# Optimization experiments

Measured on AMD Instinct MI355X. Metric: run time of the kernel, lower is better.

The kernel has to match this reference:

```python
import jax, jax.numpy as jnp
import numpy as np

B, N_FIELDS, D_IN, HID, HEADS = 1024, 32, 64, 128, 4
E_PER_G = 256
N_TOTAL = B * N_FIELDS


def setup_inputs() -> dict:
    key = jax.random.key(0)
    ks = jax.random.split(key, 12)
    # per-graph template edges, replicated with per-graph node offsets
    src_t = jax.random.randint(ks[0], (E_PER_G,), 0, N_FIELDS)
    dst_t = jax.random.randint(ks[1], (E_PER_G,), 0, N_FIELDS)
    offs = (jnp.arange(B) * N_FIELDS)[:, None]
    src = (src_t[None, :] + offs).reshape(-1)
    dst = (dst_t[None, :] + offs).reshape(-1)
    loops = jnp.arange(N_TOTAL)  # PyG GATConv add_self_loops=True
    edge_index = jnp.stack([jnp.concatenate([src, loops]),
                            jnp.concatenate([dst, loops])]).astype(jnp.int32)
    batch_idx = jnp.repeat(jnp.arange(B), N_FIELDS).astype(jnp.int32)

    def glorot(k, shape):
        fan = shape[0]
        return jax.random.normal(k, shape, jnp.float32) / np.float32(np.sqrt(fan))

    return {
        "x_fields": jax.random.normal(ks[2], (B, N_FIELDS, D_IN), jnp.float32),
        "aligner_w": glorot(ks[3], (D_IN, HID)),
        "aligner_b": jnp.zeros((HID,), jnp.float32),
        "ln_gamma": jnp.ones((HID,), jnp.float32),
        "ln_beta": jnp.zeros((HID,), jnp.float32),
        "gate_logits": jnp.full((N_FIELDS,), 2.2, jnp.float32),
        "w1": glorot(ks[4], (HID, HEADS * HID)),
        "att_src1": jax.random.normal(ks[5], (HEADS, HID), jnp.float32) * 0.1,
        "att_dst1": jax.random.normal(ks[6], (HEADS, HID), jnp.float32) * 0.1,
        "bias1": jnp.zeros((HEADS * HID,), jnp.float32),
        "w2": glorot(ks[7], (HEADS * HID, HID)),
        "att_src2": jax.random.normal(ks[8], (1, HID), jnp.float32) * 0.1,
        "att_dst2": jax.random.normal(ks[9], (1, HID), jnp.float32) * 0.1,
        "bias2": jnp.zeros((HID,), jnp.float32),
        "edge_index": edge_index,
        "batch_idx": batch_idx,
    }


def _gat(x, W, a_src, a_dst, bias, src, dst, heads, out_dim, concat):
    n = x.shape[0]
    h = (x @ W).reshape(n, heads, out_dim)          # [N,H,F]
    e_s = jnp.einsum('nhf,hf->nh', h, a_src)         # per-node src logits
    e_d = jnp.einsum('nhf,hf->nh', h, a_dst)
    logits = jax.nn.leaky_relu(e_s[src] + e_d[dst], 0.2)   # [E,H]
    # segment softmax over destination nodes (self-loops -> no empty segs)
    m = jax.ops.segment_max(logits, dst, num_segments=n)
    ex = jnp.exp(logits - m[dst])
    denom = jax.ops.segment_sum(ex, dst, num_segments=n)
    alpha = ex / denom[dst]
    out = jax.ops.segment_sum(h[src] * alpha[..., None], dst, num_segments=n)
    out = out.reshape(n, heads * out_dim) if concat else out.mean(axis=1)
    return out + bias


def reference(x_fields, aligner_w, aligner_b, ln_gamma, ln_beta, gate_logits,
              w1, att_src1, att_dst1, bias1, w2, att_src2, att_dst2, bias2,
              edge_index, batch_idx):
    # fused alignment: one Linear over all fields
    aligned = x_fields @ aligner_w + aligner_b       # [B,N,HID]
    mu = aligned.mean(-1, keepdims=True)
    var = ((aligned - mu) ** 2).mean(-1, keepdims=True)
    normed = (aligned - mu) / jnp.sqrt(var + 1e-5) * ln_gamma + ln_beta
    gate = jax.nn.sigmoid(gate_logits)               # [N]
    x = (normed * gate[None, :, None]).reshape(-1, HID)  # [B*N, HID]
    src, dst = edge_index[0], edge_index[1]
    x = _gat(x, w1, att_src1, att_dst1, bias1, src, dst, HEADS, HID, True)
    x = jax.nn.elu(x)
    x = _gat(x, w2, att_src2, att_dst2, bias2, src, dst, 1, HID, False)
    counts = jax.ops.segment_sum(jnp.ones((x.shape[0],), x.dtype), batch_idx,
                                 num_segments=B)
    graph_embedding = jax.ops.segment_sum(x, batch_idx, num_segments=B) / counts[:, None]
    return graph_embedding, gate
```

## Files before the change

kernel.cpp:

```cpp
#include <hip/hip_runtime.h>
#include <hip/hip_bf16.h>
#include <cstdint>
#include <cstddef>

#define NB    1024
#define NF    32
#define DIN   64
#define HID   128
#define HEADS 4
#define NTOT  (NB*NF)
#define H1DIM (HEADS*HID)

typedef __attribute__((ext_vector_type(8))) short          bf16x8;
typedef __attribute__((ext_vector_type(8))) unsigned short u16x8;
typedef __attribute__((ext_vector_type(4))) float          f32x4;

__device__ __forceinline__ float bf2f(unsigned short u) {
    return __uint_as_float(((unsigned)u) << 16);
}
__device__ __forceinline__ unsigned short f2bf(float f) {
    unsigned u = __float_as_uint(f);
    return (unsigned short)((u + 0x7FFF + ((u >> 16) & 1)) >> 16);
}

__global__ __launch_bounds__(256) void k_prep(
    const float* __restrict__ w1, const float* __restrict__ w2,
    const float* __restrict__ Wa,
    unsigned short* __restrict__ w1T, unsigned short* __restrict__ w2T,
    unsigned short* __restrict__ WaT)
{
    int i = blockIdx.x * 256 + threadIdx.x;
    if (i < HID * H1DIM) {
        int n = i >> 7, k = i & 127;
        w1T[i] = f2bf(w1[k * H1DIM + n]);
    } else if (i < 2 * HID * H1DIM) {
        int j = i - HID * H1DIM;
        int n = j >> 9, k = j & 511;
        w2T[j] = f2bf(w2[k * HID + n]);
    } else {
        int j = i - 2 * HID * H1DIM;
        int c = j >> 6, k = j & 63;
        WaT[j] = f2bf(Wa[k * HID + c]);
    }
}

__global__ __launch_bounds__(256, 2) void k_mega(
    const float* __restrict__ xf, const unsigned short* __restrict__ WaT,
    const float* __restrict__ ba, const float* __restrict__ gamma,
    const float* __restrict__ beta, const float* __restrict__ gl,
    const unsigned short* __restrict__ w1T, const float* __restrict__ as1,
    const float* __restrict__ ad1, const float* __restrict__ b1,
    const unsigned short* __restrict__ w2T, const float* __restrict__ as2,
    const float* __restrict__ ad2, const float* __restrict__ b2,
    const int* __restrict__ src, const int* __restrict__ dst, int epg,
    float* __restrict__ dout)
{
    __shared__ char S[72192];
    unsigned short* h1T    = (unsigned short*)S;
    unsigned short* x1L    = (unsigned short*)S;
    unsigned short* alphaL = (unsigned short*)(S + 40960);
    unsigned short* x0L    = (unsigned short*)(S + 51200);
    int*   cntL  = (int*)  (S + 59904);
    float* lnS   = (float*)(S + 64000);
    float* lnS2  = (float*)(S + 64512);
    float* esL   = (float*)(S + 65024);
    float* edL   = (float*)(S + 65536);
    float* rsumL = (float*)(S + 66048);
    float* es2p  = (float*)(S + 66560);
    float* ed2p  = (float*)(S + 67072);
    float* aL2   = (float*)(S + 67584);
    float* sc2   = (float*)(S + 71808);

    const int b = blockIdx.x, t = threadIdx.x;
    const int l = t & 63, w = t >> 6;
    const int g = l >> 4, i16 = l & 15;
    const int nb = b * NF;
    const f32x4 zf4 = {0.f, 0.f, 0.f, 0.f};

    for (int i = t; i < NF * NF; i += 256) cntL[i] = 0;
    __syncthreads();
    for (int i = t; i < epg; i += 256) {
        int sv = src[b * epg + i] - nb;
        int dv = dst[b * epg + i] - nb;
        atomicAdd(&cntL[dv * NF + sv], 1);
    }
    if (t < NF) atomicAdd(&cntL[t * NF + t], 1);

    f32x4 accA[2][2];
    #pragma unroll
    for (int m = 0; m < 2; ++m)
        #pragma unroll
        for (int n = 0; n < 2; ++n) accA[m][n] = zf4;

    #pragma unroll
    for (int k = 0; k < 2; ++k) {
        bf16x8 aF[2];
        #pragma unroll
        for (int m = 0; m < 2; ++m) {
            const float* p = &xf[(size_t)(nb + m * 16 + i16) * DIN + k * 32 + g * 8];
            float4 f0 = *(const float4*)p;
            float4 f1 = *(const float4*)(p + 4);
            u16x8 v;
            v[0] = f2bf(f0.x); v[1] = f2bf(f0.y); v[2] = f2bf(f0.z); v[3] = f2bf(f0.w);
            v[4] = f2bf(f1.x); v[5] = f2bf(f1.y); v[6] = f2bf(f1.z); v[7] = f2bf(f1.w);
            aF[m] = (bf16x8)v;
        }
        #pragma unroll
        for (int n = 0; n < 2; ++n) {
            bf16x8 bF = *(const bf16x8*)&WaT[(size_t)(w * 32 + n * 16 + i16) * DIN + k * 32 + g * 8];
            #pragma unroll
            for (int m = 0; m < 2; ++m)
                accA[m][n] = __builtin_amdgcn_mfma_f32_16x16x32_bf16(aF[m], bF, accA[m][n], 0, 0, 0);
        }
    }
    float val[2][2][4];
    float bav[2];
    #pragma unroll
    for (int n = 0; n < 2; ++n) bav[n] = ba[w * 32 + n * 16 + i16];
    float ps[2][4], ps2[2][4];
    #pragma unroll
    for (int m = 0; m < 2; ++m)
        #pragma unroll
        for (int v = 0; v < 4; ++v) {
            float a0 = accA[m][0][v] + bav[0];
            float a1 = accA[m][1][v] + bav[1];
            val[m][0][v] = a0; val[m][1][v] = a1;
            ps[m][v] = a0 + a1;
            ps2[m][v] = a0 * a0 + a1 * a1;
        }
    #pragma unroll
    for (int o = 1; o < 16; o <<= 1) {
        #pragma unroll
        for (int m = 0; m < 2; ++m)
            #pragma unroll
            for (int v = 0; v < 4; ++v) {
                ps[m][v]  += __shfl_xor(ps[m][v], o);
                ps2[m][v] += __shfl_xor(ps2[m][v], o);
            }
    }
    if (i16 == 0) {
        #pragma unroll
        for (int m = 0; m < 2; ++m)
            #pragma unroll
            for (int v = 0; v < 4; ++v) {
                int r = m * 16 + g * 4 + v;
                lnS[w * 32 + r]  = ps[m][v];
                lnS2[w * 32 + r] = ps2[m][v];
            }
    }
    __syncthreads();
    #pragma unroll
    for (int m = 0; m < 2; ++m)
        #pragma unroll
        for (int v = 0; v < 4; ++v) {
            int r = m * 16 + g * 4 + v;
            float S1 = lnS[r] + lnS[32 + r] + lnS[64 + r] + lnS[96 + r];
            float S2 = lnS2[r] + lnS2[32 + r] + lnS2[64 + r] + lnS2[96 + r];
            float mu = S1 * (1.0f / HID);
            float var = S2 * (1.0f / HID) - mu * mu;
            float rs = rsqrtf(var + 1e-5f);
            float gt = 1.0f / (1.0f + __expf(-gl[r]));
            #pragma unroll
            for (int n = 0; n < 2; ++n) {
                int c = w * 32 + n * 16 + i16;
                float xv = ((val[m][n][v] - mu) * rs * gamma[c] + beta[c]) * gt;
                x0L[r * 136 + c] = f2bf(xv);
            }
        }
    __syncthreads();

    f32x4 acc1[2][8];
    #pragma unroll
    for (int m = 0; m < 2; ++m)
        #pragma unroll
        for (int n = 0; n < 8; ++n) acc1[m][n] = zf4;

    #pragma unroll 1
    for (int k = 0; k < 4; ++k) {
        bf16x8 aF[2];
        #pragma unroll
        for (int m = 0; m < 2; ++m)
            aF[m] = *(const bf16x8*)&x0L[(m * 16 + i16) * 136 + k * 32 + g * 8];
        #pragma unroll
        for (int n = 0; n < 8; ++n) {
            bf16x8 bF = *(const bf16x8*)&w1T[(size_t)(w * 128 + n * 16 + i16) * 128 + k * 32 + g * 8];
            #pragma unroll
            for (int m = 0; m < 2; ++m)
                acc1[m][n] = __builtin_amdgcn_mfma_f32_16x16x32_bf16(aF[m], bF, acc1[m][n], 0, 0, 0);
        }
    }
    {
        float asv[8], adv[8];
        #pragma unroll
        for (int n = 0; n < 8; ++n) {
            int f = n * 16 + i16;
            asv[n] = as1[w * 128 + f];
            adv[n] = ad1[w * 128 + f];
        }
        float pe[2][4], pd[2][4];
        #pragma unroll
        for (int m = 0; m < 2; ++m)
            #pragma unroll
            for (int v = 0; v < 4; ++v) {
                float e = 0.f, d = 0.f;
                #pragma unroll
                for (int n = 0; n < 8; ++n) {
                    e = fmaf(acc1[m][n][v], asv[n], e);
                    d = fmaf(acc1[m][n][v], adv[n], d);
                }
                pe[m][v] = e; pd[m][v] = d;
            }
        #pragma unroll
        for (int o = 1; o < 16; o <<= 1) {
            #pragma unroll
            for (int m = 0; m < 2; ++m)
                #pragma unroll
                for (int v = 0; v < 4; ++v) {
                    pe[m][v] += __shfl_xor(pe[m][v], o);
                    pd[m][v] += __shfl_xor(pd[m][v], o);
                }
        }
        if (i16 == 0) {
            #pragma unroll
            for (int m = 0; m < 2; ++m)
                #pragma unroll
                for (int v = 0; v < 4; ++v) {
                    int r = m * 16 + g * 4 + v;
                    esL[w * 32 + r] = pe[m][v];
                    edL[w * 32 + r] = pd[m][v];
                }
        }
        #pragma unroll
        for (int m = 0; m < 2; ++m)
            #pragma unroll
            for (int n = 0; n < 8; ++n) {
                int c = w * 128 + n * 16 + i16;
                unsigned d0 = (unsigned)f2bf(acc1[m][n][0]) | ((unsigned)f2bf(acc1[m][n][1]) << 16);
                unsigned d1 = (unsigned)f2bf(acc1[m][n][2]) | ((unsigned)f2bf(acc1[m][n][3]) << 16);
                uint2 pk = {d0, d1};
                *(uint2*)&h1T[c * 40 + m * 16 + g * 4] = pk;
            }
    }
    __syncthreads();

    if (t < 128) {
        int d = t >> 2, h = t & 3;
        float edv = edL[h * 32 + d];
        float mx = -INFINITY;
        #pragma unroll
        for (int s = 0; s < NF; ++s) {
            if (cntL[d * NF + s]) {
                float lg = esL[h * 32 + s] + edv;
                lg = fmaxf(lg, 0.2f * lg);
                mx = fmaxf(mx, lg);
            }
        }
        float sum = 0.f;
        #pragma unroll
        for (int s = 0; s < NF; ++s) {
            int c = cntL[d * NF + s];
            float a = 0.f;
            if (c) {
                float lg = esL[h * 32 + s] + edv;
                lg = fmaxf(lg, 0.2f * lg);
                a = (float)c * __expf(lg - mx);
                sum += a;
            }
            alphaL[(h * 32 + d) * 40 + s] = f2bf(a);
        }
        rsumL[h * 32 + d] = 1.0f / sum;
    }
    __syncthreads();

    f32x4 po[2][8];
    {
        bf16x8 aF2[2];
        #pragma unroll
        for (int m = 0; m < 2; ++m)
            aF2[m] = *(const bf16x8*)&alphaL[(w * 32 + m * 16 + i16) * 40 + g * 8];
        #pragma unroll
        for (int n = 0; n < 8; ++n) {
            bf16x8 bF = *(const bf16x8*)&h1T[(w * 128 + n * 16 + i16) * 40 + g * 8];
            #pragma unroll
            for (int m = 0; m < 2; ++m)
                po[m][n] = __builtin_amdgcn_mfma_f32_16x16x32_bf16(aF2[m], bF, zf4, 0, 0, 0);
        }
    }
    __syncthreads();
    #pragma unroll
    for (int m = 0; m < 2; ++m)
        #pragma unroll
        for (int n = 0; n < 8; ++n) {
            int c = w * 128 + n * 16 + i16;
            float bias = b1[c];
            #pragma unroll
            for (int v = 0; v < 4; ++v) {
                int r = m * 16 + g * 4 + v;
                float x = po[m][n][v] * rsumL[w * 32 + r] + bias;
                x = (x > 0.f) ? x : expm1f(x);
                x1L[r * 520 + c] = f2bf(x);
            }
        }
    __syncthreads();

    f32x4 acc2[2][2];
    #pragma unroll
    for (int m = 0; m < 2; ++m)
        #pragma unroll
        for (int n = 0; n < 2; ++n) acc2[m][n] = zf4;

    #pragma unroll 1
    for (int k = 0; k < 16; ++k) {
        bf16x8 aF[2];
        #pragma unroll
        for (int m = 0; m < 2; ++m)
            aF[m] = *(const bf16x8*)&x1L[(m * 16 + i16) * 520 + k * 32 + g * 8];
        #pragma unroll
        for (int n = 0; n < 2; ++n) {
            bf16x8 bF = *(const bf16x8*)&w2T[(size_t)(w * 32 + n * 16 + i16) * 512 + k * 32 + g * 8];
            #pragma unroll
            for (int m = 0; m < 2; ++m)
                acc2[m][n] = __builtin_amdgcn_mfma_f32_16x16x32_bf16(aF[m], bF, acc2[m][n], 0, 0, 0);
        }
    }
    {
        float a2v[2], d2v[2];
        #pragma unroll
        for (int n = 0; n < 2; ++n) {
            int c = w * 32 + n * 16 + i16;
            a2v[n] = as2[c]; d2v[n] = ad2[c];
        }
        float pe[2][4], pd[2][4];
        #pragma unroll
        for (int m = 0; m < 2; ++m)
            #pragma unroll
            for (int v = 0; v < 4; ++v) {
                float e = 0.f, d = 0.f;
                #pragma unroll
                for (int n = 0; n < 2; ++n) {
                    e = fmaf(acc2[m][n][v], a2v[n], e);
                    d = fmaf(acc2[m][n][v], d2v[n], d);
                }
                pe[m][v] = e; pd[m][v] = d;
            }
        #pragma unroll
        for (int o = 1; o < 16; o <<= 1) {
            #pragma unroll
            for (int m = 0; m < 2; ++m)
                #pragma unroll
                for (int v = 0; v < 4; ++v) {
                    pe[m][v] += __shfl_xor(pe[m][v], o);
                    pd[m][v] += __shfl_xor(pd[m][v], o);
                }
        }
        if (i16 == 0) {
            #pragma unroll
            for (int m = 0; m < 2; ++m)
                #pragma unroll
                for (int v = 0; v < 4; ++v) {
                    int r = m * 16 + g * 4 + v;
                    es2p[w * 32 + r] = pe[m][v];
                    ed2p[w * 32 + r] = pd[m][v];
                }
        }
    }
    __syncthreads();

    float* es2L = sc2;
    float* ed2L = sc2 + 32;
    float* wn2  = sc2 + 64;
    if (t < NF) {
        es2L[t] = es2p[t] + es2p[32 + t] + es2p[64 + t] + es2p[96 + t];
        ed2L[t] = ed2p[t] + ed2p[32 + t] + ed2p[64 + t] + ed2p[96 + t];
    }
    __syncthreads();
    if (t < NF) {
        int d = t;
        float edv = ed2L[d];
        float mx = -INFINITY;
        #pragma unroll
        for (int s = 0; s < NF; ++s) {
            if (cntL[d * NF + s]) {
                float lg = es2L[s] + edv;
                lg = fmaxf(lg, 0.2f * lg);
                mx = fmaxf(mx, lg);
            }
        }
        float sum = 0.f;
        #pragma unroll
        for (int s = 0; s < NF; ++s) {
            int c = cntL[d * NF + s];
            float a = 0.f;
            if (c) {
                float lg = es2L[s] + edv;
                lg = fmaxf(lg, 0.2f * lg);
                a = (float)c * __expf(lg - mx);
                sum += a;
            }
            aL2[d * 33 + s] = a;
        }
        float rs = 1.0f / sum;
        #pragma unroll
        for (int s = 0; s < NF; ++s) aL2[d * 33 + s] *= rs;
    }
    __syncthreads();
    if (t < NF) {
        float a = 0.f;
        #pragma unroll
        for (int d = 0; d < NF; ++d) a += aL2[d * 33 + t];
        wn2[t] = a;
    }
    __syncthreads();

    {
        float wr_[2][4];
        #pragma unroll
        for (int m = 0; m < 2; ++m)
            #pragma unroll
            for (int v = 0; v < 4; ++v) wr_[m][v] = wn2[m * 16 + g * 4 + v];
        float pl[2];
        #pragma unroll
        for (int n = 0; n < 2; ++n) {
            float a = 0.f;
            #pragma unroll
            for (int m = 0; m < 2; ++m)
                #pragma unroll
                for (int v = 0; v < 4; ++v)
                    a = fmaf(wr_[m][v], acc2[m][n][v], a);
            pl[n] = a;
        }
        #pragma unroll
        for (int n = 0; n < 2; ++n) {
            pl[n] += __shfl_xor(pl[n], 16);
            pl[n] += __shfl_xor(pl[n], 32);
        }
        if (l < 16) {
            #pragma unroll
            for (int n = 0; n < 2; ++n) {
                int c = w * 32 + n * 16 + l;
                dout[(size_t)b * HID + c] = pl[n] * (1.0f / NF) + b2[c];
            }
        }
    }
    if (b == 0 && t < NF)
        dout[(size_t)NB * HID + t] = 1.0f / (1.0f + __expf(-gl[t]));
}

extern "C" void kernel_launch(void* const* d_in, const int* in_sizes, int n_in,
                              void* d_out, int out_size, void* d_ws, size_t ws_size,
                              hipStream_t stream)
{
    const float* xf    = (const float*)d_in[0];
    const float* Wa    = (const float*)d_in[1];
    const float* ba    = (const float*)d_in[2];
    const float* gamma = (const float*)d_in[3];
    const float* beta  = (const float*)d_in[4];
    const float* gl    = (const float*)d_in[5];
    const float* w1    = (const float*)d_in[6];
    const float* as1   = (const float*)d_in[7];
    const float* ad1   = (const float*)d_in[8];
    const float* b1    = (const float*)d_in[9];
    const float* w2    = (const float*)d_in[10];
    const float* as2   = (const float*)d_in[11];
    const float* ad2   = (const float*)d_in[12];
    const float* b2    = (const float*)d_in[13];
    const int*   eidx  = (const int*)d_in[14];
    const int E = in_sizes[14] / 2;
    const int* srcG = eidx;
    const int* dstG = eidx + E;
    const int epg = (E - NTOT) / NB;

    char* w = (char*)d_ws;
    unsigned short* w1T = (unsigned short*)w; w += (size_t)H1DIM * HID * 2;
    unsigned short* w2T = (unsigned short*)w; w += (size_t)HID * H1DIM * 2;
    unsigned short* WaT = (unsigned short*)w; w += (size_t)HID * DIN * 2;

    k_prep<<<(2 * HID * H1DIM + DIN * HID) / 256, 256, 0, stream>>>(
        w1, w2, Wa, w1T, w2T, WaT);

    k_mega<<<NB, 256, 0, stream>>>(
        xf, WaT, ba, gamma, beta, gl, w1T, as1, ad1, b1,
        w2T, as2, ad2, b2, srcG, dstG, epg, (float*)d_out);
}
```

Baseline: 165.5 us.

## Shrink LDS footprint with XOR swizzles and byte edge counts for three blocks per CU

```diff
diff --git a/kernel.cpp b/kernel.cpp
--- a/kernel.cpp
+++ b/kernel.cpp
@@ -21,6 +21,19 @@
 __device__ __forceinline__ unsigned short f2bf(float f) {
     unsigned u = __float_as_uint(f);
     return (unsigned short)((u + 0x7FFF + ((u >> 16) & 1)) >> 16);
+}
+
+__device__ __forceinline__ int x0_at(int r, int c) {
+    return r * 128 + ((((c >> 3) ^ (r & 7)) & 15) << 3) + (c & 7);
+}
+__device__ __forceinline__ int h1_at(int f, int s) {
+    return f * 32 + ((((s >> 3) ^ ((f >> 1) & 3)) & 3) << 3) + (s & 7);
+}
+__device__ __forceinline__ int x1_at(int r, int c) {
+    return r * 512 + ((((c >> 3) ^ ((r >> 1) & 7)) & 63) << 3) + (c & 7);
+}
+__device__ __forceinline__ int al_at(int rr, int s) {
+    return rr * 32 + ((((s >> 3) ^ ((rr >> 1) & 3)) & 3) << 3) + (s & 7);
 }
 
 __global__ __launch_bounds__(256) void k_prep(
@@ -44,7 +57,7 @@
     }
 }
 
-__global__ __launch_bounds__(256, 2) void k_mega(
+__global__ __launch_bounds__(256, 3) void k_mega(
     const float* __restrict__ xf, const unsigned short* __restrict__ WaT,
     const float* __restrict__ ba, const float* __restrict__ gamma,
     const float* __restrict__ beta, const float* __restrict__ gl,
@@ -55,21 +68,22 @@
     const int* __restrict__ src, const int* __restrict__ dst, int epg,
     float* __restrict__ dout)
 {
-    __shared__ char S[72192];
+    __shared__ __align__(16) char S[54144];
+    int*            cntI   = (int*)S;
     unsigned short* h1T    = (unsigned short*)S;
     unsigned short* x1L    = (unsigned short*)S;
-    unsigned short* alphaL = (unsigned short*)(S + 40960);
-    unsigned short* x0L    = (unsigned short*)(S + 51200);
-    int*   cntL  = (int*)  (S + 59904);
-    float* lnS   = (float*)(S + 64000);
-    float* lnS2  = (float*)(S + 64512);
-    float* esL   = (float*)(S + 65024);
-    float* edL   = (float*)(S + 65536);
-    float* rsumL = (float*)(S + 66048);
-    float* es2p  = (float*)(S + 66560);
-    float* ed2p  = (float*)(S + 67072);
-    float* aL2   = (float*)(S + 67584);
-    float* sc2   = (float*)(S + 71808);
+    unsigned short* alphaL = (unsigned short*)(S + 32768);
+    unsigned short* x0L    = (unsigned short*)(S + 40960);
+    float*          aL2    = (float*)(S + 40960);
+    unsigned char*  cntB   = (unsigned char*)(S + 49152);
+    float* lnS   = (float*)(S + 50176);
+    float* lnS2  = (float*)(S + 50688);
+    float* esL   = (float*)(S + 51200);
+    float* edL   = (float*)(S + 51712);
+    float* rsumL = (float*)(S + 52224);
+    float* es2p  = (float*)(S + 52736);
+    float* ed2p  = (float*)(S + 53248);
+    float* sc2   = (float*)(S + 53760);
 
     const int b = blockIdx.x, t = threadIdx.x;
     const int l = t & 63, w = t >> 6;
@@ -77,14 +91,20 @@
     const int nb = b * NF;
     const f32x4 zf4 = {0.f, 0.f, 0.f, 0.f};
 
-    for (int i = t; i < NF * NF; i += 256) cntL[i] = 0;
+    for (int i = t; i < NF * NF; i += 256) cntI[i] = 0;
     __syncthreads();
     for (int i = t; i < epg; i += 256) {
         int sv = src[b * epg + i] - nb;
         int dv = dst[b * epg + i] - nb;
-        atomicAdd(&cntL[dv * NF + sv], 1);
-    }
-    if (t < NF) atomicAdd(&cntL[t * NF + t], 1);
+        atomicAdd(&cntI[dv * NF + sv], 1);
+    }
+    if (t < NF) atomicAdd(&cntI[t * NF + t], 1);
+    __syncthreads();
+    for (int i = t; i < NF * NF; i += 256) {
+        int c = cntI[i];
+        cntB[i] = (unsigned char)(c > 255 ? 255 : c);
+    }
+    __syncthreads();
 
     f32x4 accA[2][2];
     #pragma unroll
@@ -164,7 +184,7 @@
             for (int n = 0; n < 2; ++n) {
                 int c = w * 32 + n * 16 + i16;
                 float xv = ((val[m][n][v] - mu) * rs * gamma[c] + beta[c]) * gt;
-                x0L[r * 136 + c] = f2bf(xv);
+                x0L[x0_at(r, c)] = f2bf(xv);
             }
         }
     __syncthreads();
@@ -175,12 +195,12 @@
         #pragma unroll
         for (int n = 0; n < 8; ++n) acc1[m][n] = zf4;
 
-    #pragma unroll 1
+    #pragma unroll 2
     for (int k = 0; k < 4; ++k) {
         bf16x8 aF[2];
         #pragma unroll
         for (int m = 0; m < 2; ++m)
-            aF[m] = *(const bf16x8*)&x0L[(m * 16 + i16) * 136 + k * 32 + g * 8];
+            aF[m] = *(const bf16x8*)&x0L[x0_at(m * 16 + i16, k * 32 + g * 8)];
         #pragma unroll
         for (int n = 0; n < 8; ++n) {
             bf16x8 bF = *(const bf16x8*)&w1T[(size_t)(w * 128 + n * 16 + i16) * 128 + k * 32 + g * 8];
@@ -234,11 +254,12 @@
         for (int m = 0; m < 2; ++m)
             #pragma unroll
             for (int n = 0; n < 8; ++n) {
-                int c = w * 128 + n * 16 + i16;
+                int f = w * 128 + n * 16 + i16;
+                int s0 = m * 16 + g * 4;
                 unsigned d0 = (unsigned)f2bf(acc1[m][n][0]) | ((unsigned)f2bf(acc1[m][n][1]) << 16);
                 unsigned d1 = (unsigned)f2bf(acc1[m][n][2]) | ((unsigned)f2bf(acc1[m][n][3]) << 16);
                 uint2 pk = {d0, d1};
-                *(uint2*)&h1T[c * 40 + m * 16 + g * 4] = pk;
+                *(uint2*)&h1T[h1_at(f, s0)] = pk;
             }
     }
     __syncthreads();
@@ -249,7 +270,7 @@
         float mx = -INFINITY;
         #pragma unroll
         for (int s = 0; s < NF; ++s) {
-            if (cntL[d * NF + s]) {
+            if (cntB[d * NF + s]) {
                 float lg = esL[h * 32 + s] + edv;
                 lg = fmaxf(lg, 0.2f * lg);
                 mx = fmaxf(mx, lg);
@@ -258,7 +279,7 @@
         float sum = 0.f;
         #pragma unroll
         for (int s = 0; s < NF; ++s) {
-            int c = cntL[d * NF + s];
+            int c = cntB[d * NF + s];
             float a = 0.f;
             if (c) {
                 float lg = esL[h * 32 + s] + edv;
@@ -266,7 +287,7 @@
                 a = (float)c * __expf(lg - mx);
                 sum += a;
             }
-            alphaL[(h * 32 + d) * 40 + s] = f2bf(a);
+            alphaL[al_at(h * 32 + d, s)] = f2bf(a);
         }
         rsumL[h * 32 + d] = 1.0f / sum;
     }
@@ -277,10 +298,10 @@
         bf16x8 aF2[2];
         #pragma unroll
         for (int m = 0; m < 2; ++m)
-            aF2[m] = *(const bf16x8*)&alphaL[(w * 32 + m * 16 + i16) * 40 + g * 8];
+            aF2[m] = *(const bf16x8*)&alphaL[al_at(w * 32 + m * 16 + i16, g * 8)];
         #pragma unroll
         for (int n = 0; n < 8; ++n) {
-            bf16x8 bF = *(const bf16x8*)&h1T[(w * 128 + n * 16 + i16) * 40 + g * 8];
+            bf16x8 bF = *(const bf16x8*)&h1T[h1_at(w * 128 + n * 16 + i16, g * 8)];
             #pragma unroll
             for (int m = 0; m < 2; ++m)
                 po[m][n] = __builtin_amdgcn_mfma_f32_16x16x32_bf16(aF2[m], bF, zf4, 0, 0, 0);
@@ -297,8 +318,8 @@
             for (int v = 0; v < 4; ++v) {
                 int r = m * 16 + g * 4 + v;
                 float x = po[m][n][v] * rsumL[w * 32 + r] + bias;
-                x = (x > 0.f) ? x : expm1f(x);
-                x1L[r * 520 + c] = f2bf(x);
+                x = (x > 0.f) ? x : (__expf(x) - 1.0f);
+                x1L[x1_at(r, c)] = f2bf(x);
             }
         }
     __syncthreads();
@@ -309,12 +330,12 @@
         #pragma unroll
         for (int n = 0; n < 2; ++n) acc2[m][n] = zf4;
 
-    #pragma unroll 1
+    #pragma unroll 4
     for (int k = 0; k < 16; ++k) {
         bf16x8 aF[2];
         #pragma unroll
         for (int m = 0; m < 2; ++m)
-            aF[m] = *(const bf16x8*)&x1L[(m * 16 + i16) * 520 + k * 32 + g * 8];
+            aF[m] = *(const bf16x8*)&x1L[x1_at(m * 16 + i16, k * 32 + g * 8)];
         #pragma unroll
         for (int n = 0; n < 2; ++n) {
             bf16x8 bF = *(const bf16x8*)&w2T[(size_t)(w * 32 + n * 16 + i16) * 512 + k * 32 + g * 8];
@@ -380,7 +401,7 @@
         float mx = -INFINITY;
         #pragma unroll
         for (int s = 0; s < NF; ++s) {
-            if (cntL[d * NF + s]) {
+            if (cntB[d * NF + s]) {
                 float lg = es2L[s] + edv;
                 lg = fmaxf(lg, 0.2f * lg);
                 mx = fmaxf(mx, lg);
@@ -389,7 +410,7 @@
         float sum = 0.f;
         #pragma unroll
         for (int s = 0; s < NF; ++s) {
-            int c = cntL[d * NF + s];
+            int c = cntB[d * NF + s];
             float a = 0.f;
             if (c) {
                 float lg = es2L[s] + edv;
```

Result: faster. 158.8 us (-4.1%).
